# Performance work log

Measured on AMD Instinct MI355X. Metric: run time of the kernel, lower is better.

## Reference

```python
import jax, jax.numpy as jnp
import numpy as np

B, L, D, DP = 64, 4096, 512, 64


def setup_inputs() -> dict:
    key = jax.random.key(0)
    ks = jax.random.split(key, 7)
    s = 0.02
    return {
        "source": jax.random.normal(ks[0], (B, D), jnp.float32),
        "main_embs": jax.random.normal(ks[1], (L, B, D), jnp.float32),   # time-major memory bank
        "pos_embs": jax.random.normal(ks[2], (L, B, DP), jnp.float32),
        "W_main_in": jax.random.normal(ks[3], (D, D), jnp.float32) * s,  # main_scorer.linear_in (no bias)
        "W_pos_in": jax.random.normal(ks[4], (D, DP), jnp.float32) * s,  # pos_scorer.linear_in (no bias)
        "W_out": jax.random.normal(ks[5], (D, 2 * D), jnp.float32) * s,  # linear_out (no bias, attn_type!='mlp')
        "memory_lengths": jnp.maximum(jax.random.randint(ks[6], (B,), 1, L + 1), 1),
    }


def reference(source, main_embs, pos_embs, W_main_in, W_pos_in, W_out, memory_lengths):
    # to batch-major: (B, L, D) / (B, L, DP)
    me = jnp.transpose(main_embs, (1, 0, 2))
    pe = jnp.transpose(pos_embs, (1, 0, 2))

    # 'general' scorer: project context then dot with query (qrs_len == 1)
    mc = jnp.einsum("bld,ed->ble", me, W_main_in)          # (B, L, D)
    main_align = jnp.einsum("bd,bld->bl", source, mc)      # (B, L)
    pc = jnp.einsum("blp,dp->bld", pe, W_pos_in)           # (B, L, D)
    pos_align = jnp.einsum("bd,bld->bl", source, pc)       # (B, L)

    # length mask + softmax on each branch
    mask = jnp.arange(me.shape[1])[None, :] < memory_lengths[:, None]  # (B, L)
    neg_inf = jnp.float32(-jnp.inf)
    ma = jax.nn.softmax(jnp.where(mask, main_align, neg_inf), axis=-1)
    pa = jax.nn.softmax(jnp.where(mask, pos_align, neg_inf), axis=-1)

    # elementwise combine + renormalize
    av = ma * pa
    av = av / jnp.sum(av, axis=-1, keepdims=True)

    # context vector + output projection + tanh
    c_t = jnp.einsum("bl,bld->bd", av, me)                 # (B, D)
    concat_c = jnp.concatenate([c_t, source], axis=-1)     # (B, 2D)
    attn_h = jnp.tanh(concat_c @ W_out.T)                  # (B, D)

    return attn_h, av, ma, pa
```

## Files before the change

kernel.cpp:

```cpp
#include <hip/hip_runtime.h>
#include <cstddef>

#define NB 64
#define NL 4096
#define ND 512
#define NDP 64
#define LC 64
#define NLC (NL / LC)
#define NSLOT 4096

typedef float v2f __attribute__((ext_vector_type(2)));

__device__ __forceinline__ v2f fma2(v2f a, v2f b, v2f c) {
    return __builtin_elementwise_fma(a, b, c);
}

__global__ void __launch_bounds__(128) queries_plan_kernel(
    const float* __restrict__ source, const float* __restrict__ Wmi,
    const float* __restrict__ Wpi, const int* __restrict__ lens,
    float* __restrict__ qpm, float* __restrict__ qpp,
    int* __restrict__ table)
{
    if (blockIdx.x == NB * 4) {
        if (threadIdx.x < 64) {
            const int lane = threadIdx.x;
            const int nc = (lens[lane] + LC - 1) >> 6;
            int pre = nc;
            #pragma unroll
            for (int off = 1; off < 64; off <<= 1) {
                const int v = __shfl_up(pre, off);
                if (lane >= off) pre += v;
            }
            const int start = pre - nc;
            for (int j = 0; j < nc; ++j) table[start + j] = (lane << 6) | j;
            const int T = __shfl(pre, 63);
            for (int s = T + lane; s < NSLOT; s += 64) table[s] = -1;
        }
        return;
    }

    __shared__ float s[128];
    const int b  = blockIdx.x >> 2;
    const int eq = blockIdx.x & 3;
    const int t  = threadIdx.x;
    const int e0 = eq * 128;
    s[t] = source[b * ND + e0 + t];
    __syncthreads();

    const int d0 = t * 4;
    float4 a0 = {0,0,0,0}, a1 = {0,0,0,0};
    #pragma unroll 4
    for (int e = 0; e < 128; e += 2) {
        const float4 w0 = *(const float4*)(Wmi + (size_t)(e0 + e) * ND + d0);
        const float4 w1 = *(const float4*)(Wmi + (size_t)(e0 + e + 1) * ND + d0);
        const float x0 = s[e], x1 = s[e + 1];
        a0.x = fmaf(x0, w0.x, a0.x); a0.y = fmaf(x0, w0.y, a0.y);
        a0.z = fmaf(x0, w0.z, a0.z); a0.w = fmaf(x0, w0.w, a0.w);
        a1.x = fmaf(x1, w1.x, a1.x); a1.y = fmaf(x1, w1.y, a1.y);
        a1.z = fmaf(x1, w1.z, a1.z); a1.w = fmaf(x1, w1.w, a1.w);
    }
    a0.x += a1.x; a0.y += a1.y; a0.z += a1.z; a0.w += a1.w;
    *(float4*)(qpm + (size_t)(b * 4 + eq) * ND + d0) = a0;

    if (t < NDP) {
        float c0 = 0.f, c1 = 0.f;
        #pragma unroll 4
        for (int e = 0; e < 128; e += 2) {
            c0 = fmaf(s[e],     Wpi[(size_t)(e0 + e) * NDP + t],     c0);
            c1 = fmaf(s[e + 1], Wpi[(size_t)(e0 + e + 1) * NDP + t], c1);
        }
        qpp[(b * 4 + eq) * NDP + t] = c0 + c1;
    }
}

__global__ void __launch_bounds__(256) pass1_kernel(
    const float* __restrict__ me, const float* __restrict__ pe,
    const float* __restrict__ qpm, const float* __restrict__ qpp,
    const int* __restrict__ mem_len, const int* __restrict__ table,
    float* __restrict__ a_main, float* __restrict__ a_pos,
    float* __restrict__ Sbuf, float* __restrict__ MZ)
{
    __shared__ __align__(16) float qp_lds[4][NDP];
    const int lane = threadIdx.x & 63;
    const int wid  = threadIdx.x >> 6;
    const int task = table[blockIdx.x * 4 + wid];
    if (task < 0) return;
    const int b  = task >> 6;
    const int lc = task & 63;

    const int len  = mem_len[b];
    const int l0   = lc * LC;
    const int nrow = min(LC, len - l0);

    float4 q0 = {0,0,0,0}, q1 = {0,0,0,0};
    float qp = 0.f;
    #pragma unroll
    for (int eq = 0; eq < 4; ++eq) {
        const float4* qr = (const float4*)(qpm + (size_t)(b * 4 + eq) * ND);
        const float4 u0 = qr[lane], u1 = qr[64 + lane];
        q0.x += u0.x; q0.y += u0.y; q0.z += u0.z; q0.w += u0.w;
        q1.x += u1.x; q1.y += u1.y; q1.z += u1.z; q1.w += u1.w;
        qp += qpp[(b * 4 + eq) * NDP + lane];
    }
    qp_lds[wid][lane] = qp;

    float accp = 0.f;
    {
        const float4* pr = (const float4*)(pe + ((size_t)(l0 + lane) * NB + b) * NDP);
        #pragma unroll
        for (int k = 0; k < 16; ++k) {
            const float4 pv = pr[k];
            const float4 qv = *(const float4*)&qp_lds[wid][k * 4];
            accp = fmaf(pv.x, qv.x, accp);
            accp = fmaf(pv.y, qv.y, accp);
            accp = fmaf(pv.z, qv.z, accp);
            accp = fmaf(pv.w, qv.w, accp);
        }
        if (lane < nrow) a_pos[(size_t)b * NL + l0 + lane] = accp;
    }
    const int accp_i = __float_as_int(accp);

    const size_t rstride = (size_t)NB * ND;
    const float* rp = me + ((size_t)l0 * NB + b) * ND;
    const float* rp1 = rp + ((nrow > 1) ? rstride : 0);
    float4 c0 = ((const float4*)rp)[lane];
    float4 c1 = ((const float4*)rp)[64 + lane];
    float4 d0 = ((const float4*)rp1)[lane];
    float4 d1 = ((const float4*)rp1)[64 + lane];

    float m = -1e30f, Z = 0.f, keep = 0.f;
    v2f S0 = {0,0}, S1 = {0,0}, S2 = {0,0}, S3 = {0,0};

    for (int i = 0; i < nrow; ++i) {
        const float* np = rp + ((i + 2 < nrow) ? 2 * rstride : 0);
        const float4 n0 = ((const float4*)np)[lane];
        const float4 n1 = ((const float4*)np)[64 + lane];

        v2f dd = {0.f, 0.f};
        dd = fma2((v2f){c0.x, c0.y}, (v2f){q0.x, q0.y}, dd);
        dd = fma2((v2f){c0.z, c0.w}, (v2f){q0.z, q0.w}, dd);
        dd = fma2((v2f){c1.x, c1.y}, (v2f){q1.x, q1.y}, dd);
        dd = fma2((v2f){c1.z, c1.w}, (v2f){q1.z, q1.w}, dd);
        float accm = dd.x + dd.y;
        #pragma unroll
        for (int off = 32; off; off >>= 1)
            accm += __shfl_xor(accm, off);

        keep = (lane == i) ? accm : keep;
        const float ap = __int_as_float(__builtin_amdgcn_readlane(accp_i, i));
        const float sv = accm + ap;

        if (sv > m) {
            const float sc = __expf(m - sv);
            const v2f sc2 = {sc, sc};
            Z = fmaf(Z, sc, 1.f);
            S0 = fma2(S0, sc2, (v2f){c0.x, c0.y});
            S1 = fma2(S1, sc2, (v2f){c0.z, c0.w});
            S2 = fma2(S2, sc2, (v2f){c1.x, c1.y});
            S3 = fma2(S3, sc2, (v2f){c1.z, c1.w});
            m = sv;
        } else {
            const float w = __expf(sv - m);
            const v2f w2 = {w, w};
            Z += w;
            S0 = fma2((v2f){c0.x, c0.y}, w2, S0);
            S1 = fma2((v2f){c0.z, c0.w}, w2, S1);
            S2 = fma2((v2f){c1.x, c1.y}, w2, S2);
            S3 = fma2((v2f){c1.z, c1.w}, w2, S3);
        }
        c0 = d0; c1 = d1; d0 = n0; d1 = n1;
        rp += rstride;
    }

    if (lane < nrow) a_main[(size_t)b * NL + l0 + lane] = keep;

    float* sp = Sbuf + ((size_t)b * NLC + lc) * ND;
    ((float4*)sp)[lane]      = (float4){S0.x, S0.y, S1.x, S1.y};
    ((float4*)sp)[64 + lane] = (float4){S2.x, S2.y, S3.x, S3.y};
    if (lane == 0) {
        MZ[2 * (b * NLC + lc)]     = m;
        MZ[2 * (b * NLC + lc) + 1] = Z;
    }
}

__global__ void __launch_bounds__(1024) stats_finalize_kernel(
    const float* __restrict__ MZ, const int* __restrict__ mem_len,
    float* __restrict__ ma_io, float* __restrict__ pa_io,
    float* __restrict__ out_av, float* __restrict__ coef)
{
    __shared__ float red[16][6];
    __shared__ float bc[6];
    const int b = blockIdx.x;
    const int tid = threadIdx.x;
    const int lane = tid & 63, wid = tid >> 6;
    const int len = mem_len[b];

    float va[4], vp[4];
    float Am = -1e30f, Pm = -1e30f, Cm = -1e30f;
    #pragma unroll
    for (int k = 0; k < 4; ++k) {
        const int l = tid + k * 1024;
        va[k] = ma_io[(size_t)b * NL + l];
        vp[k] = pa_io[(size_t)b * NL + l];
        if (l < len) {
            Am = fmaxf(Am, va[k]);
            Pm = fmaxf(Pm, vp[k]);
            Cm = fmaxf(Cm, va[k] + vp[k]);
        }
    }
    #pragma unroll
    for (int off = 32; off; off >>= 1) {
        Am = fmaxf(Am, __shfl_xor(Am, off));
        Pm = fmaxf(Pm, __shfl_xor(Pm, off));
        Cm = fmaxf(Cm, __shfl_xor(Cm, off));
    }
    if (lane == 0) { red[wid][0] = Am; red[wid][1] = Pm; red[wid][2] = Cm; }
    __syncthreads();
    if (tid < 16) {
        float a = red[tid][0], p = red[tid][1], c = red[tid][2];
        #pragma unroll
        for (int off = 8; off; off >>= 1) {
            a = fmaxf(a, __shfl_xor(a, off));
            p = fmaxf(p, __shfl_xor(p, off));
            c = fmaxf(c, __shfl_xor(c, off));
        }
        if (tid == 0) { bc[0] = a; bc[1] = p; bc[2] = c; }
    }
    __syncthreads();
    const float MA = bc[0], MP = bc[1], MC = bc[2];

    float Az = 0.f, Pz = 0.f, Cz = 0.f;
    #pragma unroll
    for (int k = 0; k < 4; ++k) {
        const int l = tid + k * 1024;
        if (l < len) {
            Az += __expf(va[k] - MA);
            Pz += __expf(vp[k] - MP);
            Cz += __expf(va[k] + vp[k] - MC);
        }
    }
    #pragma unroll
    for (int off = 32; off; off >>= 1) {
        Az += __shfl_xor(Az, off);
        Pz += __shfl_xor(Pz, off);
        Cz += __shfl_xor(Cz, off);
    }
    if (lane == 0) { red[wid][3] = Az; red[wid][4] = Pz; red[wid][5] = Cz; }
    __syncthreads();
    if (tid < 16) {
        float a = red[tid][3], p = red[tid][4], c = red[tid][5];
        #pragma unroll
        for (int off = 8; off; off >>= 1) {
            a += __shfl_xor(a, off);
            p += __shfl_xor(p, off);
            c += __shfl_xor(c, off);
        }
        if (tid == 0) { bc[3] = a; bc[4] = p; bc[5] = c; }
    }
    __syncthreads();
    const float iA = 1.f / bc[3], iP = 1.f / bc[4], iC = 1.f / bc[5];

    if (tid < NLC) {
        const int nv = (len + LC - 1) >> 6;
        const float mlc = MZ[2 * (b * NLC + tid)];
        coef[b * NLC + tid] = (tid < nv) ? __expf(mlc - MC) * iC : 0.f;
    }

    #pragma unroll
    for (int k = 0; k < 4; ++k) {
        const int l = tid + k * 1024;
        const bool v = l < len;
        const size_t idx = (size_t)b * NL + l;
        ma_io[idx]  = v ? __expf(va[k] - MA) * iA : 0.f;
        pa_io[idx]  = v ? __expf(vp[k] - MP) * iP : 0.f;
        out_av[idx] = v ? __expf(va[k] + vp[k] - MC) * iC : 0.f;
    }
}

__global__ void __launch_bounds__(256) ctx_kernel(
    const float* __restrict__ Sbuf, const float* __restrict__ coef,
    const int* __restrict__ mem_len, float* __restrict__ c_t)
{
    __shared__ float sh[3][64];
    const int b = blockIdx.x >> 3, dseg = blockIdx.x & 7;
    const int dl = threadIdx.x & 63, k = threadIdx.x >> 6;
    const int d = dseg * 64 + dl;
    const int nv = (mem_len[b] + LC - 1) >> 6;
    float acc = 0.f;
    for (int lcc = k; lcc < nv; lcc += 4)
        acc = fmaf(coef[b * NLC + lcc],
                   Sbuf[((size_t)b * NLC + lcc) * ND + d], acc);
    if (k) sh[k - 1][dl] = acc;
    __syncthreads();
    if (k == 0)
        c_t[b * ND + d] = acc + sh[0][dl] + sh[1][dl] + sh[2][dl];
}

__global__ void __launch_bounds__(256) out_kernel(
    const float* __restrict__ c_t, const float* __restrict__ source,
    const float* __restrict__ Wout, float* __restrict__ attn_h)
{
    __shared__ float cs[2 * ND];
    const int b = blockIdx.x >> 3;
    const int eg = blockIdx.x & 7;
    const int tid = threadIdx.x;

    for (int d = tid; d < ND; d += 256) {
        cs[d] = c_t[b * ND + d];
        cs[ND + d] = source[b * ND + d];
    }
    __syncthreads();

    const int wid = tid >> 6, lane = tid & 63;
    const float4* csv = (const float4*)cs;
    for (int e = eg * 64 + wid; e < eg * 64 + 64; e += 4) {
        const float4* wrow = (const float4*)(Wout + (size_t)e * 2 * ND);
        float acc = 0.f;
        #pragma unroll
        for (int j = 0; j < 4; ++j) {
            const float4 w = wrow[lane + 64 * j];
            const float4 c = csv[lane + 64 * j];
            acc += w.x * c.x + w.y * c.y + w.z * c.z + w.w * c.w;
        }
        #pragma unroll
        for (int off = 32; off; off >>= 1) acc += __shfl_xor(acc, off);
        if (lane == 0) attn_h[(size_t)b * ND + e] = tanhf(acc);
    }
}

extern "C" void kernel_launch(void* const* d_in, const int* in_sizes, int n_in,
                              void* d_out, int out_size, void* d_ws, size_t ws_size,
                              hipStream_t stream)
{
    const float* source = (const float*)d_in[0];
    const float* me     = (const float*)d_in[1];
    const float* pe     = (const float*)d_in[2];
    const float* Wmi    = (const float*)d_in[3];
    const float* Wpi    = (const float*)d_in[4];
    const float* Wout   = (const float*)d_in[5];
    const int*   lens   = (const int*)d_in[6];

    float* out    = (float*)d_out;
    float* attn_h = out;
    float* av     = attn_h + NB * ND;
    float* ma     = av + NB * NL;
    float* pa     = ma + NB * NL;

    float* ws    = (float*)d_ws;
    float* qpm   = ws;
    float* qpp   = qpm + NB * 4 * ND;
    float* Sbuf  = qpp + NB * 4 * NDP;
    float* MZ    = Sbuf + (size_t)NB * NLC * ND;
    float* coef  = MZ + NB * NLC * 2;
    float* c_t   = coef + NB * NLC;
    int*   table = (int*)(c_t + NB * ND);

    queries_plan_kernel   <<<NB * 4 + 1, 128, 0, stream>>>(source, Wmi, Wpi,
                                                           lens, qpm, qpp, table);
    pass1_kernel          <<<NSLOT / 4, 256, 0, stream>>>(me, pe, qpm, qpp, lens,
                                                          table, ma, pa, Sbuf, MZ);
    stats_finalize_kernel <<<NB, 1024, 0, stream>>>(MZ, lens, ma, pa, av, coef);
    ctx_kernel            <<<NB * 8, 256, 0, stream>>>(Sbuf, coef, lens, c_t);
    out_kernel            <<<NB * 8, 256, 0, stream>>>(c_t, source, Wout, attn_h);
}
```

Baseline: 115.2 us.

## Batch pass1 rows in groups of four with double-buffered loads; fuse ctx into stats

The pass1 main loop now processes four memory rows per step. Their dot products are computed together and their butterfly shuffles interleaved, while the next four rows load into a second register buffer. This raises memory-level parallelism and cuts serialized shuffle latency, at the cost of more registers; launch bounds now request 4 blocks per CU. The separate ctx kernel is folded into the stats kernel, with chunk coefficients kept in LDS, removing one launch and the global coef round trip. The ctx reduction now runs on only 128 threads per batch row, with fewer blocks. A leftover dead block computing an unused prow remains.

```diff
diff --git a/kernel.cpp b/kernel.cpp
--- a/kernel.cpp
+++ b/kernel.cpp
@@ -73,7 +73,7 @@
     }
 }
 
-__global__ void __launch_bounds__(256) pass1_kernel(
+__global__ void __launch_bounds__(256, 4) pass1_kernel(
     const float* __restrict__ me, const float* __restrict__ pe,
     const float* __restrict__ qpm, const float* __restrict__ qpp,
     const int* __restrict__ mem_len, const int* __restrict__ table,
@@ -91,6 +91,8 @@
     const int len  = mem_len[b];
     const int l0   = lc * LC;
     const int nrow = min(LC, len - l0);
+    const int nr4  = (nrow + 3) & ~3;
+    const int last = nrow - 1;
 
     float4 q0 = {0,0,0,0}, q1 = {0,0,0,0};
     float qp = 0.f;
@@ -106,7 +108,11 @@
 
     float accp = 0.f;
     {
-        const float4* pr = (const float4*)(pe + ((size_t)(l0 + lane) * NB + b) * NDP);
+        const int prow = l0 + (lane & 31) ? l0 + (lane & 63) : l0;
+    }
+    {
+        const int prow = l0 + min(lane, last);
+        const float4* pr = (const float4*)(pe + ((size_t)prow * NB + b) * NDP);
         #pragma unroll
         for (int k = 0; k < 16; ++k) {
             const float4 pv = pr[k];
@@ -121,55 +127,86 @@
     const int accp_i = __float_as_int(accp);
 
     const size_t rstride = (size_t)NB * ND;
-    const float* rp = me + ((size_t)l0 * NB + b) * ND;
-    const float* rp1 = rp + ((nrow > 1) ? rstride : 0);
-    float4 c0 = ((const float4*)rp)[lane];
-    float4 c1 = ((const float4*)rp)[64 + lane];
-    float4 d0 = ((const float4*)rp1)[lane];
-    float4 d1 = ((const float4*)rp1)[64 + lane];
+    const float* base = me + ((size_t)l0 * NB + b) * ND;
 
     float m = -1e30f, Z = 0.f, keep = 0.f;
     v2f S0 = {0,0}, S1 = {0,0}, S2 = {0,0}, S3 = {0,0};
 
-    for (int i = 0; i < nrow; ++i) {
-        const float* np = rp + ((i + 2 < nrow) ? 2 * rstride : 0);
-        const float4 n0 = ((const float4*)np)[lane];
-        const float4 n1 = ((const float4*)np)[64 + lane];
-
-        v2f dd = {0.f, 0.f};
-        dd = fma2((v2f){c0.x, c0.y}, (v2f){q0.x, q0.y}, dd);
-        dd = fma2((v2f){c0.z, c0.w}, (v2f){q0.z, q0.w}, dd);
-        dd = fma2((v2f){c1.x, c1.y}, (v2f){q1.x, q1.y}, dd);
-        dd = fma2((v2f){c1.z, c1.w}, (v2f){q1.z, q1.w}, dd);
-        float accm = dd.x + dd.y;
-        #pragma unroll
-        for (int off = 32; off; off >>= 1)
-            accm += __shfl_xor(accm, off);
-
-        keep = (lane == i) ? accm : keep;
-        const float ap = __int_as_float(__builtin_amdgcn_readlane(accp_i, i));
-        const float sv = accm + ap;
-
-        if (sv > m) {
-            const float sc = __expf(m - sv);
-            const v2f sc2 = {sc, sc};
-            Z = fmaf(Z, sc, 1.f);
-            S0 = fma2(S0, sc2, (v2f){c0.x, c0.y});
-            S1 = fma2(S1, sc2, (v2f){c0.z, c0.w});
-            S2 = fma2(S2, sc2, (v2f){c1.x, c1.y});
-            S3 = fma2(S3, sc2, (v2f){c1.z, c1.w});
-            m = sv;
-        } else {
-            const float w = __expf(sv - m);
-            const v2f w2 = {w, w};
-            Z += w;
-            S0 = fma2((v2f){c0.x, c0.y}, w2, S0);
-            S1 = fma2((v2f){c0.z, c0.w}, w2, S1);
-            S2 = fma2((v2f){c1.x, c1.y}, w2, S2);
-            S3 = fma2((v2f){c1.z, c1.w}, w2, S3);
-        }
-        c0 = d0; c1 = d1; d0 = n0; d1 = n1;
-        rp += rstride;
+    float4 A[4][2], B[4][2];
+
+    auto process = [&](float4 R[4][2], int i0) {
+        float acc[4];
+        #pragma unroll
+        for (int j = 0; j < 4; ++j) {
+            v2f dd = {0.f, 0.f};
+            dd = fma2((v2f){R[j][0].x, R[j][0].y}, (v2f){q0.x, q0.y}, dd);
+            dd = fma2((v2f){R[j][0].z, R[j][0].w}, (v2f){q0.z, q0.w}, dd);
+            dd = fma2((v2f){R[j][1].x, R[j][1].y}, (v2f){q1.x, q1.y}, dd);
+            dd = fma2((v2f){R[j][1].z, R[j][1].w}, (v2f){q1.z, q1.w}, dd);
+            acc[j] = dd.x + dd.y;
+        }
+        #pragma unroll
+        for (int off = 32; off; off >>= 1) {
+            #pragma unroll
+            for (int j = 0; j < 4; ++j)
+                acc[j] += __shfl_xor(acc[j], off);
+        }
+        #pragma unroll
+        for (int j = 0; j < 4; ++j) {
+            const int row = i0 + j;
+            keep = (lane == row) ? acc[j] : keep;
+            const float ap = __int_as_float(
+                __builtin_amdgcn_readlane(accp_i, min(row, last)));
+            const float sv = (row < nrow) ? acc[j] + ap : -1e30f;
+            if (sv > m) {
+                const float sc = __expf(m - sv);
+                const v2f sc2 = {sc, sc};
+                Z = fmaf(Z, sc, 1.f);
+                S0 = fma2(S0, sc2, (v2f){R[j][0].x, R[j][0].y});
+                S1 = fma2(S1, sc2, (v2f){R[j][0].z, R[j][0].w});
+                S2 = fma2(S2, sc2, (v2f){R[j][1].x, R[j][1].y});
+                S3 = fma2(S3, sc2, (v2f){R[j][1].z, R[j][1].w});
+                m = sv;
+            } else {
+                const float w = __expf(sv - m);
+                const v2f w2 = {w, w};
+                Z += w;
+                S0 = fma2((v2f){R[j][0].x, R[j][0].y}, w2, S0);
+                S1 = fma2((v2f){R[j][0].z, R[j][0].w}, w2, S1);
+                S2 = fma2((v2f){R[j][1].x, R[j][1].y}, w2, S2);
+                S3 = fma2((v2f){R[j][1].z, R[j][1].w}, w2, S3);
+            }
+        }
+    };
+
+    #pragma unroll
+    for (int j = 0; j < 4; ++j) {
+        const float* p = base + (size_t)min(j, last) * rstride;
+        A[j][0] = ((const float4*)p)[lane];
+        A[j][1] = ((const float4*)p)[64 + lane];
+    }
+
+    int i = 0;
+    for (;;) {
+        #pragma unroll
+        for (int j = 0; j < 4; ++j) {
+            const float* p = base + (size_t)min(i + 4 + j, last) * rstride;
+            B[j][0] = ((const float4*)p)[lane];
+            B[j][1] = ((const float4*)p)[64 + lane];
+        }
+        process(A, i);
+        i += 4;
+        if (i >= nr4) break;
+
+        #pragma unroll
+        for (int j = 0; j < 4; ++j) {
+            const float* p = base + (size_t)min(i + 4 + j, last) * rstride;
+            A[j][0] = ((const float4*)p)[lane];
+            A[j][1] = ((const float4*)p)[64 + lane];
+        }
+        process(B, i);
+        i += 4;
+        if (i >= nr4) break;
     }
 
     if (lane < nrow) a_main[(size_t)b * NL + l0 + lane] = keep;
@@ -183,13 +220,15 @@
     }
 }
 
-__global__ void __launch_bounds__(1024) stats_finalize_kernel(
-    const float* __restrict__ MZ, const int* __restrict__ mem_len,
+__global__ void __launch_bounds__(1024) stats_ctx_kernel(
+    const float* __restrict__ MZ, const float* __restrict__ Sbuf,
+    const int* __restrict__ mem_len,
     float* __restrict__ ma_io, float* __restrict__ pa_io,
-    float* __restrict__ out_av, float* __restrict__ coef)
+    float* __restrict__ out_av, float* __restrict__ c_t)
 {
     __shared__ float red[16][6];
     __shared__ float bc[6];
+    __shared__ float coef_s[NLC];
     const int b = blockIdx.x;
     const int tid = threadIdx.x;
     const int lane = tid & 63, wid = tid >> 6;
@@ -259,11 +298,11 @@
     }
     __syncthreads();
     const float iA = 1.f / bc[3], iP = 1.f / bc[4], iC = 1.f / bc[5];
+    const int nv = (len + LC - 1) >> 6;
 
     if (tid < NLC) {
-        const int nv = (len + LC - 1) >> 6;
         const float mlc = MZ[2 * (b * NLC + tid)];
-        coef[b * NLC + tid] = (tid < nv) ? __expf(mlc - MC) * iC : 0.f;
+        coef_s[tid] = (tid < nv) ? __expf(mlc - MC) * iC : 0.f;
     }
 
     #pragma unroll
@@ -275,25 +314,21 @@
         pa_io[idx]  = v ? __expf(vp[k] - MP) * iP : 0.f;
         out_av[idx] = v ? __expf(va[k] + vp[k] - MC) * iC : 0.f;
     }
-}
-
-__global__ void __launch_bounds__(256) ctx_kernel(
-    const float* __restrict__ Sbuf, const float* __restrict__ coef,
-    const int* __restrict__ mem_len, float* __restrict__ c_t)
-{
-    __shared__ float sh[3][64];
-    const int b = blockIdx.x >> 3, dseg = blockIdx.x & 7;
-    const int dl = threadIdx.x & 63, k = threadIdx.x >> 6;
-    const int d = dseg * 64 + dl;
-    const int nv = (mem_len[b] + LC - 1) >> 6;
-    float acc = 0.f;
-    for (int lcc = k; lcc < nv; lcc += 4)
-        acc = fmaf(coef[b * NLC + lcc],
-                   Sbuf[((size_t)b * NLC + lcc) * ND + d], acc);
-    if (k) sh[k - 1][dl] = acc;
-    __syncthreads();
-    if (k == 0)
-        c_t[b * ND + d] = acc + sh[0][dl] + sh[1][dl] + sh[2][dl];
+    __syncthreads();
+
+    if (tid < 128) {
+        float4 acc = {0.f, 0.f, 0.f, 0.f};
+        for (int lcc = 0; lcc < nv; ++lcc) {
+            const float cf = coef_s[lcc];
+            const float4 sv4 =
+                ((const float4*)(Sbuf + ((size_t)b * NLC + lcc) * ND))[tid];
+            acc.x = fmaf(cf, sv4.x, acc.x);
+            acc.y = fmaf(cf, sv4.y, acc.y);
+            acc.z = fmaf(cf, sv4.z, acc.z);
+            acc.w = fmaf(cf, sv4.w, acc.w);
+        }
+        ((float4*)(c_t + b * ND))[tid] = acc;
+    }
 }
 
 __global__ void __launch_bounds__(256) out_kernel(
@@ -351,15 +386,13 @@
     float* qpp   = qpm + NB * 4 * ND;
     float* Sbuf  = qpp + NB * 4 * NDP;
     float* MZ    = Sbuf + (size_t)NB * NLC * ND;
-    float* coef  = MZ + NB * NLC * 2;
-    float* c_t   = coef + NB * NLC;
+    float* c_t   = MZ + NB * NLC * 2;
     int*   table = (int*)(c_t + NB * ND);
 
-    queries_plan_kernel   <<<NB * 4 + 1, 128, 0, stream>>>(source, Wmi, Wpi,
-                                                           lens, qpm, qpp, table);
-    pass1_kernel          <<<NSLOT / 4, 256, 0, stream>>>(me, pe, qpm, qpp, lens,
-                                                          table, ma, pa, Sbuf, MZ);
-    stats_finalize_kernel <<<NB, 1024, 0, stream>>>(MZ, lens, ma, pa, av, coef);
-    ctx_kernel            <<<NB * 8, 256, 0, stream>>>(Sbuf, coef, lens, c_t);
-    out_kernel            <<<NB * 8, 256, 0, stream>>>(c_t, source, Wout, attn_h);
-}
+    queries_plan_kernel<<<NB * 4 + 1, 128, 0, stream>>>(source, Wmi, Wpi,
+                                                        lens, qpm, qpp, table);
+    pass1_kernel       <<<NSLOT / 4, 256, 0, stream>>>(me, pe, qpm, qpp, lens,
+                                                       table, ma, pa, Sbuf, MZ);
+    stats_ctx_kernel   <<<NB, 1024, 0, stream>>>(MZ, Sbuf, lens, ma, pa, av, c_t);
+    out_kernel         <<<NB * 8, 256, 0, stream>>>(c_t, source, Wout, attn_h);
+}
```

After: 115.2 us (median of 4 runs). About the same (+0.0%).
